# Optimization experiments

Hardware: AMD Instinct MI355X
Metric: run time of the kernel (lower is better)

## Reference

```python
import jax, jax.numpy as jnp
import numpy as np

N_POL, N_TICK, N_COMM = 1000, 98000, 1000
N = N_POL + N_TICK + N_COMM
E = 1000000
EMB, HID, OUT, HEADS = 32, 64, 32, 4
EDGE_DIM = 5
N_STATES, N_SECTORS, N_INDUSTRIES = 50, 11, 74


def _p(k, shape, fan_in):
    return jax.random.normal(k, shape, jnp.float32) * (1.0 / np.sqrt(fan_in))


def setup_inputs():
    ks = jax.random.split(jax.random.key(0), 30)
    F1 = HID // HEADS
    d = {}
    d["edge_index"] = jax.random.randint(ks[0], (2, E), 0, N)
    d["edge_attr"] = jax.random.normal(ks[1], (E, EDGE_DIM), jnp.float32)
    d["pol_feat"] = jax.random.normal(ks[2], (N_POL, 7), jnp.float32)
    d["state_ids"] = jax.random.randint(ks[3], (N_POL,), 0, N_STATES)
    d["sector_ids"] = jax.random.randint(ks[4], (N_TICK,), 0, N_SECTORS)
    d["industry_ids"] = jax.random.randint(ks[5], (N_TICK,), 0, N_INDUSTRIES)
    d["comp_scalar"] = jax.random.normal(ks[6], (N_TICK, 1), jnp.float32)
    d["pol_W"] = _p(ks[7], (7, EMB), 7); d["pol_b"] = jnp.zeros((EMB,), jnp.float32)
    d["state_E"] = _p(ks[8], (N_STATES, EMB), 1)
    d["sector_E"] = _p(ks[9], (N_SECTORS, 8), 1)
    d["industry_E"] = _p(ks[10], (N_INDUSTRIES, 8), 1)
    d["comp_W"] = _p(ks[11], (17, EMB), 17); d["comp_b"] = jnp.zeros((EMB,), jnp.float32)
    d["comm_E"] = _p(ks[12], (N_COMM, EMB), 1)
    d["ln_g"] = jnp.ones((EMB,), jnp.float32); d["ln_b"] = jnp.zeros((EMB,), jnp.float32)
    d["c1_W"] = _p(ks[13], (EMB, HEADS * F1), EMB)
    d["c1_as"] = _p(ks[14], (HEADS, F1), F1); d["c1_ad"] = _p(ks[15], (HEADS, F1), F1)
    d["c1_eW"] = _p(ks[16], (EDGE_DIM, HEADS * F1), EDGE_DIM)
    d["c1_ae"] = _p(ks[17], (HEADS, F1), F1)
    d["c1_b"] = jnp.zeros((HID,), jnp.float32)
    d["c2_W"] = _p(ks[18], (HID, OUT), HID)
    d["c2_as"] = _p(ks[19], (1, OUT), OUT); d["c2_ad"] = _p(ks[20], (1, OUT), OUT)
    d["c2_eW"] = _p(ks[21], (EDGE_DIM, OUT), EDGE_DIM)
    d["c2_ae"] = _p(ks[22], (1, OUT), OUT)
    d["c2_b"] = jnp.zeros((OUT,), jnp.float32)
    return d


def _segment_softmax(logits, seg, num):
    # numerically stable per-destination softmax, per head (axis 0 is edges)
    m = jax.ops.segment_max(logits, seg, num_segments=num)
    ex = jnp.exp(logits - m[seg])
    s = jax.ops.segment_sum(ex, seg, num_segments=num)
    return ex / s[seg]


def _gat(x, src, dst, eattr, W, a_s, a_d, eW, a_e, b, heads, feat, concat):
    # PyG GATConv (eval mode): linear -> per-node alpha terms -> per-edge
    # leaky_relu -> destination softmax -> weighted scatter-sum.
    n = x.shape[0]
    h = (x @ W).reshape(n, heads, feat)                     # [N,H,F]
    a_src = jnp.sum(h * a_s, -1)                            # [N,H]
    a_dst = jnp.sum(h * a_d, -1)                            # [N,H]
    a_edge = jnp.sum((eattr @ eW).reshape(-1, heads, feat) * a_e, -1)  # [E,H]
    alpha = jax.nn.leaky_relu(a_src[src] + a_dst[dst] + a_edge, 0.2)
    alpha = _segment_softmax(alpha, dst, n)                 # [E,H]
    out = jax.ops.segment_sum(h[src] * alpha[..., None], dst, num_segments=n)
    out = out.reshape(n, heads * feat) if concat else out.mean(1)
    return out + b


def _forward(edge_index, edge_attr, pol_feat, state_ids, sector_ids, industry_ids,
             comp_scalar, pol_W, pol_b, state_E, sector_E, industry_E, comp_W,
             comp_b, comm_E, ln_g, ln_b, c1_W, c1_as, c1_ad, c1_eW, c1_ae, c1_b,
             c2_W, c2_as, c2_ad, c2_eW, c2_ae, c2_b):
    # node features
    pol = jax.nn.relu(pol_feat @ pol_W + pol_b) + state_E[state_ids]
    comp_in = jnp.concatenate([sector_E[sector_ids], industry_E[industry_ids], comp_scalar], 1)
    comp = jax.nn.relu(comp_in @ comp_W + comp_b)
    x = jnp.concatenate([pol, comp, comm_E], 0)             # [N,EMB]
    mu = jnp.mean(x, -1, keepdims=True)
    var = jnp.mean((x - mu) ** 2, -1, keepdims=True)
    x = (x - mu) / jnp.sqrt(var + 1e-5) * ln_g + ln_b
    # add self-loops with fill_value='mean' (per-dst mean of incoming edge_attr)
    src, dst = edge_index[0], edge_index[1]
    cnt = jax.ops.segment_sum(jnp.ones((E,), jnp.float32), dst, num_segments=N)
    loop_attr = jax.ops.segment_sum(edge_attr, dst, num_segments=N) / jnp.maximum(cnt, 1.0)[:, None]
    idx = jnp.arange(N)
    src2 = jnp.concatenate([src, idx]); dst2 = jnp.concatenate([dst, idx])
    ea2 = jnp.concatenate([edge_attr, loop_attr], 0)
    x = jax.nn.elu(_gat(x, src2, dst2, ea2, c1_W, c1_as, c1_ad, c1_eW, c1_ae, c1_b, HEADS, HID // HEADS, True))
    x = _gat(x, src2, dst2, ea2, c2_W, c2_as, c2_ad, c2_eW, c2_ae, c2_b, 1, OUT, False)
    return x


def reference(edge_index, edge_attr, pol_feat, state_ids, sector_ids, industry_ids,
              comp_scalar, pol_W, pol_b, state_E, sector_E, industry_E, comp_W,
              comp_b, comm_E, ln_g, ln_b, c1_W, c1_as, c1_ad, c1_eW, c1_ae, c1_b,
              c2_W, c2_as, c2_ad, c2_eW, c2_ae, c2_b):
    return _forward(edge_index, edge_attr, pol_feat, state_ids, sector_ids, industry_ids,
                    comp_scalar, pol_W, pol_b, state_E, sector_E, industry_E, comp_W,
                    comp_b, comm_E, ln_g, ln_b, c1_W, c1_as, c1_ad, c1_eW, c1_ae, c1_b,
                    c2_W, c2_as, c2_ad, c2_eW, c2_ae, c2_b)
```

## Files before the change

### kernel.cpp

```cpp
#include <hip/hip_runtime.h>
#include <math.h>

#define NPOL   1000
#define NTICK  98000
#define NCOMM  1000
#define NN     100000
#define NE     1000000
#define NE2    1100000
#define NPREBLK  1563
#define PRET     400128

__device__ __forceinline__ unsigned short f2bf(float v) {
    unsigned u = __float_as_uint(v);
    u += 0x7FFFu + ((u >> 16) & 1u);
    return (unsigned short)(u >> 16);
}
__device__ __forceinline__ float bf2f(unsigned short s) {
    return __uint_as_float(((unsigned)s) << 16);
}

__global__ void __launch_bounds__(256) k_pre(
    const int* __restrict__ ei, int* __restrict__ deg, int* __restrict__ ord,
    const float* __restrict__ pol_feat, const int* __restrict__ state_ids,
    const int* __restrict__ sector_ids, const int* __restrict__ industry_ids,
    const float* __restrict__ comp_scalar,
    const float* __restrict__ pol_W, const float* __restrict__ pol_b,
    const float* __restrict__ state_E, const float* __restrict__ sector_E,
    const float* __restrict__ industry_E, const float* __restrict__ comp_W,
    const float* __restrict__ comp_b, const float* __restrict__ comm_E,
    const float* __restrict__ ln_g, const float* __restrict__ ln_b,
    const float* __restrict__ c1_W, const float* __restrict__ c1_as,
    const float* __restrict__ c1_ad,
    unsigned short* __restrict__ h1b, float* __restrict__ as1,
    float* __restrict__ ad1) {
    __shared__ float sW1[2048];
    __shared__ float sCompW[544];
    __shared__ float sPolW[224];
    __shared__ float sAs[64], sAd[64];
    __shared__ float sLg[32], sLb[32], sPb[32], sCb[32];
    int t = threadIdx.x;
    int tid = blockIdx.x * 256 + t;
    int e0 = tid, e1 = tid + PRET, e2 = tid + 2 * PRET;
    bool b1 = e1 < NE, b2 = e2 < NE;
    int d0 = ei[NE + e0];
    int d1 = b1 ? ei[NE + e1] : 0;
    int d2 = b2 ? ei[NE + e2] : 0;
    for (int i = t; i < 2048; i += 256) sW1[i] = c1_W[i];
    for (int i = t; i < 544; i += 256) sCompW[i] = comp_W[i];
    if (t < 224) sPolW[t] = pol_W[t];
    if (t < 64) { sAs[t] = c1_as[t]; sAd[t] = c1_ad[t]; }
    if (t < 32) { sLg[t] = ln_g[t]; sLb[t] = ln_b[t]; sPb[t] = pol_b[t]; sCb[t] = comp_b[t]; }
    __syncthreads();
    int r0 = atomicAdd(&deg[d0], 1);
    int r1 = b1 ? atomicAdd(&deg[d1], 1) : 0;
    int r2 = b2 ? atomicAdd(&deg[d2], 1) : 0;
    if (tid < 4 * NN) {
        int n = tid >> 2, q = tid & 3, jb = q * 8;
        float x[8];
        if (n < NPOL) {
            float f[7];
            #pragma unroll
            for (int i = 0; i < 7; ++i) f[i] = pol_feat[n * 7 + i];
            int sid = state_ids[n];
            #pragma unroll
            for (int jj = 0; jj < 8; ++jj) {
                int j = jb + jj;
                float v = sPb[j];
                #pragma unroll
                for (int i = 0; i < 7; ++i) v += f[i] * sPolW[i * 32 + j];
                v = v > 0.f ? v : 0.f;
                x[jj] = v + state_E[sid * 32 + j];
            }
        } else if (n < NPOL + NTICK) {
            int tt = n - NPOL;
            float f[17];
            int sec = sector_ids[tt], ind = industry_ids[tt];
            #pragma unroll
            for (int i = 0; i < 8; ++i) { f[i] = sector_E[sec * 8 + i]; f[8 + i] = industry_E[ind * 8 + i]; }
            f[16] = comp_scalar[tt];
            #pragma unroll
            for (int jj = 0; jj < 8; ++jj) {
                int j = jb + jj;
                float v = sCb[j];
                #pragma unroll
                for (int i = 0; i < 17; ++i) v += f[i] * sCompW[i * 32 + j];
                x[jj] = v > 0.f ? v : 0.f;
            }
        } else {
            int c = n - (NPOL + NTICK);
            float4 a = *(const float4*)&comm_E[c * 32 + jb];
            float4 b = *(const float4*)&comm_E[c * 32 + jb + 4];
            x[0] = a.x; x[1] = a.y; x[2] = a.z; x[3] = a.w;
            x[4] = b.x; x[5] = b.y; x[6] = b.z; x[7] = b.w;
        }
        float s1 = 0.f;
        #pragma unroll
        for (int jj = 0; jj < 8; ++jj) s1 += x[jj];
        s1 += __shfl_xor(s1, 1); s1 += __shfl_xor(s1, 2);
        float mu = s1 * (1.f / 32.f);
        float s2 = 0.f;
        #pragma unroll
        for (int jj = 0; jj < 8; ++jj) { float dd = x[jj] - mu; s2 += dd * dd; }
        s2 += __shfl_xor(s2, 1); s2 += __shfl_xor(s2, 2);
        float inv = rsqrtf(s2 * (1.f / 32.f) + 1e-5f);
        #pragma unroll
        for (int jj = 0; jj < 8; ++jj) x[jj] = (x[jj] - mu) * inv * sLg[jb + jj] + sLb[jb + jj];
        float4 acc0 = {0,0,0,0}, acc1 = {0,0,0,0}, acc2 = {0,0,0,0}, acc3 = {0,0,0,0};
        int qb = (t & 63) & ~3;
        int jc = q * 16;
        #pragma unroll
        for (int p = 0; p < 4; ++p) {
            #pragma unroll
            for (int jj = 0; jj < 8; ++jj) {
                float xs = __shfl(x[jj], qb + p, 64);
                const float4* wr = (const float4*)&sW1[(p * 8 + jj) * 64 + jc];
                float4 w0 = wr[0], w1 = wr[1], w2 = wr[2], w3 = wr[3];
                acc0.x = fmaf(xs, w0.x, acc0.x); acc0.y = fmaf(xs, w0.y, acc0.y);
                acc0.z = fmaf(xs, w0.z, acc0.z); acc0.w = fmaf(xs, w0.w, acc0.w);
                acc1.x = fmaf(xs, w1.x, acc1.x); acc1.y = fmaf(xs, w1.y, acc1.y);
                acc1.z = fmaf(xs, w1.z, acc1.z); acc1.w = fmaf(xs, w1.w, acc1.w);
                acc2.x = fmaf(xs, w2.x, acc2.x); acc2.y = fmaf(xs, w2.y, acc2.y);
                acc2.z = fmaf(xs, w2.z, acc2.z); acc2.w = fmaf(xs, w2.w, acc2.w);
                acc3.x = fmaf(xs, w3.x, acc3.x); acc3.y = fmaf(xs, w3.y, acc3.y);
                acc3.z = fmaf(xs, w3.z, acc3.z); acc3.w = fmaf(xs, w3.w, acc3.w);
            }
        }
        const float4* asv = (const float4*)sAs;
        const float4* adv = (const float4*)sAd;
        float4 a0 = asv[q * 4], a1 = asv[q * 4 + 1], a2 = asv[q * 4 + 2], a3 = asv[q * 4 + 3];
        float4 b0 = adv[q * 4], b1v = adv[q * 4 + 1], b2v = adv[q * 4 + 2], b3 = adv[q * 4 + 3];
        float av = acc0.x * a0.x + acc0.y * a0.y + acc0.z * a0.z + acc0.w * a0.w
                 + acc1.x * a1.x + acc1.y * a1.y + acc1.z * a1.z + acc1.w * a1.w
                 + acc2.x * a2.x + acc2.y * a2.y + acc2.z * a2.z + acc2.w * a2.w
                 + acc3.x * a3.x + acc3.y * a3.y + acc3.z * a3.z + acc3.w * a3.w;
        float dv = acc0.x * b0.x + acc0.y * b0.y + acc0.z * b0.z + acc0.w * b0.w
                 + acc1.x * b1v.x + acc1.y * b1v.y + acc1.z * b1v.z + acc1.w * b1v.w
                 + acc2.x * b2v.x + acc2.y * b2v.y + acc2.z * b2v.z + acc2.w * b2v.w
                 + acc3.x * b3.x + acc3.y * b3.y + acc3.z * b3.z + acc3.w * b3.w;
        as1[tid] = av;
        ad1[tid] = dv;
        uint4 w1o, w2o;
        w1o.x = (unsigned)f2bf(acc0.x) | ((unsigned)f2bf(acc0.y) << 16);
        w1o.y = (unsigned)f2bf(acc0.z) | ((unsigned)f2bf(acc0.w) << 16);
        w1o.z = (unsigned)f2bf(acc1.x) | ((unsigned)f2bf(acc1.y) << 16);
        w1o.w = (unsigned)f2bf(acc1.z) | ((unsigned)f2bf(acc1.w) << 16);
        w2o.x = (unsigned)f2bf(acc2.x) | ((unsigned)f2bf(acc2.y) << 16);
        w2o.y = (unsigned)f2bf(acc2.z) | ((unsigned)f2bf(acc2.w) << 16);
        w2o.z = (unsigned)f2bf(acc3.x) | ((unsigned)f2bf(acc3.y) << 16);
        w2o.w = (unsigned)f2bf(acc3.z) | ((unsigned)f2bf(acc3.w) << 16);
        unsigned short* hp = h1b + (unsigned)n * 64u + (unsigned)jc;
        *(uint4*)hp = w1o;
        *(uint4*)(hp + 8) = w2o;
    }
    ord[e0] = r0;
    if (b1) ord[e1] = r1;
    if (b2) ord[e2] = r2;
}

__global__ void k_scan1(const int* __restrict__ deg, int* __restrict__ row_start,
                        int* __restrict__ bsum) {
    __shared__ int tmp[1024];
    int i = blockIdx.x * 1024 + threadIdx.x;
    int v = (i < NN) ? deg[i] + 1 : 0;
    tmp[threadIdx.x] = v;
    __syncthreads();
    for (int off = 1; off < 1024; off <<= 1) {
        int u = (threadIdx.x >= off) ? tmp[threadIdx.x - off] : 0;
        __syncthreads();
        tmp[threadIdx.x] += u;
        __syncthreads();
    }
    if (i < NN) row_start[i] = tmp[threadIdx.x] - v;
    if (threadIdx.x == 1023) bsum[blockIdx.x] = tmp[1023];
}
__global__ void k_scan2(int* __restrict__ bsum, int nb) {
    __shared__ int tmp[128];
    int t = threadIdx.x;
    int v = (t < nb) ? bsum[t] : 0;
    tmp[t] = v;
    __syncthreads();
    for (int off = 1; off < 128; off <<= 1) {
        int u = (t >= off) ? tmp[t - off] : 0;
        __syncthreads();
        tmp[t] += u;
        __syncthreads();
    }
    if (t < nb) bsum[t] = tmp[t] - v;
}
__global__ void k_scan3(int* __restrict__ row_start, const int* __restrict__ bsum) {
    int i = blockIdx.x * blockDim.x + threadIdx.x;
    if (i < NN) row_start[i] += bsum[i >> 10];
}

__global__ void __launch_bounds__(256) k_fill(
    const int* __restrict__ ei, const float* __restrict__ edge_attr,
    const int* __restrict__ row_start, const int* __restrict__ ord,
    const float* __restrict__ c1_eW, const float* __restrict__ c1_ae,
    const float* __restrict__ c2_eW, const float* __restrict__ c2_ae,
    float4* __restrict__ rec) {
    __shared__ float we1s[20];
    __shared__ float we2s[5];
    int t = threadIdx.x;
    if (t < 20) {
        int d = t >> 2, h = t & 3;
        float s = 0.f;
        for (int f = 0; f < 16; ++f) s += c1_eW[d * 64 + h * 16 + f] * c1_ae[h * 16 + f];
        we1s[t] = s;
    } else if (t >= 32 && t < 37) {
        int d = t - 32;
        float s = 0.f;
        for (int f = 0; f < 32; ++f) s += c2_eW[d * 32 + f] * c2_ae[f];
        we2s[d] = s;
    }
    __syncthreads();
    int e = blockIdx.x * 256 + t;
    if (e >= NE) return;
    int s = ei[e], d = ei[NE + e];
    int pos = row_start[d] + 1 + ord[e];
    float a[5];
    #pragma unroll
    for (int k = 0; k < 5; ++k) a[k] = edge_attr[e * 5 + k];
    float e0 = 0.f, e1 = 0.f, e2 = 0.f, e3 = 0.f, e4 = 0.f;
    #pragma unroll
    for (int k = 0; k < 5; ++k) {
        e0 += a[k] * we1s[k * 4 + 0];
        e1 += a[k] * we1s[k * 4 + 1];
        e2 += a[k] * we1s[k * 4 + 2];
        e3 += a[k] * we1s[k * 4 + 3];
        e4 += a[k] * we2s[k];
    }
    unsigned u01 = (unsigned)f2bf(e0) | ((unsigned)f2bf(e1) << 16);
    unsigned u23 = (unsigned)f2bf(e2) | ((unsigned)f2bf(e3) << 16);
    rec[pos] = make_float4(__int_as_float(s), __uint_as_float(u01),
                           __uint_as_float(u23), e4);
}

__global__ void __launch_bounds__(256) k_agg1(
    const int* __restrict__ row_start, const int* __restrict__ deg,
    float4* __restrict__ rec,
    const float* __restrict__ as1, const float* __restrict__ ad1,
    const unsigned short* __restrict__ h1b, const float* __restrict__ c1_b,
    unsigned short* __restrict__ x1b) {
    __shared__ float pT[4][2][32][4];
    __shared__ int   srcT[4][2][32];
    int wid = threadIdx.x >> 6;
    int lane = threadIdx.x & 63;
    int half = lane >> 5;
    int j = lane & 31;
    int h = j >> 3;
    int n = blockIdx.x * 8 + wid * 2 + half;
    int base = row_start[n];
    int dg   = deg[n];
    const float4* as1v4 = (const float4*)as1;
    const float4* ad1v4 = (const float4*)ad1;
    float4 adv = ad1v4[n];
    float4 asv = as1v4[n];
    unsigned uself = *(const unsigned*)(h1b + (unsigned)n * 64u + 2u * (unsigned)j);

    float ssum = 0.f, acc0 = 0.f, acc1 = 0.f;
    float aes0 = 0.f, aes1 = 0.f, aes2 = 0.f, aes3 = 0.f, ae2sum = 0.f;

    for (int i0 = 0; i0 < dg; i0 += 32) {
        int clen = dg - i0; if (clen > 32) clen = 32;
        int idx = i0 + j;
        if (idx < dg) {
            float4 r = rec[base + 1 + idx];
            int s = __float_as_int(r.x);
            unsigned u01 = __float_as_uint(r.y), u23 = __float_as_uint(r.z);
            float ae0  = bf2f((unsigned short)u01);
            float ae1v = bf2f((unsigned short)(u01 >> 16));
            float ae2v = bf2f((unsigned short)u23);
            float ae3v = bf2f((unsigned short)(u23 >> 16));
            float4 av = as1v4[s];
            float l0 = av.x + adv.x + ae0;  l0 = l0 > 0.f ? l0 : 0.2f * l0;
            float l1 = av.y + adv.y + ae1v; l1 = l1 > 0.f ? l1 : 0.2f * l1;
            float l2 = av.z + adv.z + ae2v; l2 = l2 > 0.f ? l2 : 0.2f * l2;
            float l3 = av.w + adv.w + ae3v; l3 = l3 > 0.f ? l3 : 0.2f * l3;
            float4 q = make_float4(__expf(l0), __expf(l1), __expf(l2), __expf(l3));
            *(float4*)&pT[wid][half][j][0] = q;
            srcT[wid][half][j] = s;
            aes0 += ae0; aes1 += ae1v; aes2 += ae2v; aes3 += ae3v;
            ae2sum += r.w;
        }
        int i = 0;
        for (; i + 4 <= clen; i += 4) {
            int s0 = srcT[wid][half][i],     s1 = srcT[wid][half][i + 1];
            int s2 = srcT[wid][half][i + 2], s3 = srcT[wid][half][i + 3];
            float q0 = pT[wid][half][i][h],     q1 = pT[wid][half][i + 1][h];
            float q2 = pT[wid][half][i + 2][h], q3 = pT[wid][half][i + 3][h];
            unsigned g0 = *(const unsigned*)(h1b + (unsigned)s0 * 64u + 2u * (unsigned)j);
            unsigned g1 = *(const unsigned*)(h1b + (unsigned)s1 * 64u + 2u * (unsigned)j);
            unsigned g2 = *(const unsigned*)(h1b + (unsigned)s2 * 64u + 2u * (unsigned)j);
            unsigned g3 = *(const unsigned*)(h1b + (unsigned)s3 * 64u + 2u * (unsigned)j);
            ssum += (q0 + q1) + (q2 + q3);
            acc0 = fmaf(q0, bf2f((unsigned short)g0),
                   fmaf(q1, bf2f((unsigned short)g1),
                   fmaf(q2, bf2f((unsigned short)g2),
                   fmaf(q3, bf2f((unsigned short)g3), acc0))));
            acc1 = fmaf(q0, bf2f((unsigned short)(g0 >> 16)),
                   fmaf(q1, bf2f((unsigned short)(g1 >> 16)),
                   fmaf(q2, bf2f((unsigned short)(g2 >> 16)),
                   fmaf(q3, bf2f((unsigned short)(g3 >> 16)), acc1))));
        }
        for (; i < clen; ++i) {
            int s0 = srcT[wid][half][i];
            float q0 = pT[wid][half][i][h];
            unsigned g0 = *(const unsigned*)(h1b + (unsigned)s0 * 64u + 2u * (unsigned)j);
            ssum += q0;
            acc0 = fmaf(q0, bf2f((unsigned short)g0), acc0);
            acc1 = fmaf(q0, bf2f((unsigned short)(g0 >> 16)), acc1);
        }
    }
    #pragma unroll
    for (int m = 1; m < 32; m <<= 1) {
        aes0 += __shfl_xor(aes0, m);
        aes1 += __shfl_xor(aes1, m);
        aes2 += __shfl_xor(aes2, m);
        aes3 += __shfl_xor(aes3, m);
        ae2sum += __shfl_xor(ae2sum, m);
    }
    float invd = 1.f / fmaxf((float)dg, 1.f);
    float aesh = (h == 0) ? aes0 : (h == 1) ? aes1 : (h == 2) ? aes2 : aes3;
    float adh  = (h == 0) ? adv.x : (h == 1) ? adv.y : (h == 2) ? adv.z : adv.w;
    float ash  = (h == 0) ? asv.x : (h == 1) ? asv.y : (h == 2) ? asv.z : asv.w;
    float ls = ash + adh + aesh * invd;
    ls = ls > 0.f ? ls : 0.2f * ls;
    float ps = __expf(ls);
    ssum += ps;
    acc0 = fmaf(ps, bf2f((unsigned short)uself), acc0);
    acc1 = fmaf(ps, bf2f((unsigned short)(uself >> 16)), acc1);
    if (j == 0) {
        rec[base] = make_float4(__int_as_float(n), 0.f, 0.f, ae2sum * invd);
    }
    float inv_s = 1.f / ssum;
    float x0 = acc0 * inv_s + c1_b[2 * j];
    float x1 = acc1 * inv_s + c1_b[2 * j + 1];
    x0 = (x0 > 0.f) ? x0 : (__expf(x0) - 1.f);
    x1 = (x1 > 0.f) ? x1 : (__expf(x1) - 1.f);
    unsigned w = (unsigned)f2bf(x0) | ((unsigned)f2bf(x1) << 16);
    *(unsigned*)(x1b + (unsigned)n * 64u + 2u * (unsigned)j) = w;
}

__global__ void __launch_bounds__(256) k_mid(
    const unsigned short* __restrict__ x1b, const float* __restrict__ c2_W,
    const float* __restrict__ c2_as, const float* __restrict__ c2_ad,
    unsigned short* __restrict__ h2b, float* __restrict__ as2,
    float* __restrict__ ad2) {
    int wave = (blockIdx.x * 256 + threadIdx.x) >> 6;
    int lane = threadIdx.x & 63;
    int half = lane >> 5, j = lane & 31;
    int n = wave * 2 + half;
    unsigned u = *(const unsigned*)(x1b + (unsigned)n * 64u + j * 2u);
    float acc = 0.f;
    #pragma unroll
    for (int t = 0; t < 32; ++t) {
        unsigned xu = (unsigned)__shfl((int)u, half * 32 + t, 64);
        float x0 = bf2f((unsigned short)xu);
        float x1 = bf2f((unsigned short)(xu >> 16));
        acc = fmaf(x0, c2_W[(2 * t) * 32 + j], acc);
        acc = fmaf(x1, c2_W[(2 * t + 1) * 32 + j], acc);
    }
    float a = acc * c2_as[j], b = acc * c2_ad[j];
    #pragma unroll
    for (int m = 16; m > 0; m >>= 1) {
        a += __shfl_xor(a, m, 64);
        b += __shfl_xor(b, m, 64);
    }
    if (j == 0) { as2[n] = a; ad2[n] = b; }
    h2b[(unsigned)n * 32u + j] = f2bf(acc);
}

__global__ void __launch_bounds__(256) k_agg2(
    const int* __restrict__ row_start, const int* __restrict__ deg,
    const float4* __restrict__ rec, const float* __restrict__ as2,
    const float* __restrict__ ad2, const unsigned short* __restrict__ h2b,
    const float* __restrict__ c2_b, float* __restrict__ out) {
    __shared__ float2 spT[8][32];
    int t = threadIdx.x;
    int half = t >> 5;
    int l32 = t & 31;
    int n = blockIdx.x * 8 + half;
    int base = row_start[n];
    int len = deg[n] + 1;
    float ad2n = ad2[n];
    float ssum = 0.f, acc = 0.f;
    for (int i0 = 0; i0 < len; i0 += 32) {
        int clen = len - i0; if (clen > 32) clen = 32;
        int idx = i0 + l32;
        float p = 0.f; int s = 0;
        if (idx < len) {
            float4 r = rec[base + idx];
            s = __float_as_int(r.x);
            float l = as2[s] + ad2n + r.w;
            l = l > 0.f ? l : 0.2f * l;
            p = __expf(l);
        }
        ssum += p;
        spT[half][l32] = make_float2(__int_as_float(s), p);
        int i = 0;
        for (; i + 4 <= clen; i += 4) {
            float2 e0 = spT[half][i],     e1 = spT[half][i + 1];
            float2 e2 = spT[half][i + 2], e3 = spT[half][i + 3];
            int s0 = __float_as_int(e0.x), s1 = __float_as_int(e1.x);
            int s2 = __float_as_int(e2.x), s3 = __float_as_int(e3.x);
            float g0 = bf2f(h2b[(unsigned)s0 * 32u + l32]);
            float g1 = bf2f(h2b[(unsigned)s1 * 32u + l32]);
            float g2 = bf2f(h2b[(unsigned)s2 * 32u + l32]);
            float g3 = bf2f(h2b[(unsigned)s3 * 32u + l32]);
            acc = fmaf(e0.y, g0, fmaf(e1.y, g1, fmaf(e2.y, g2, fmaf(e3.y, g3, acc))));
        }
        for (; i < clen; ++i) {
            float2 e0 = spT[half][i];
            int s0 = __float_as_int(e0.x);
            acc = fmaf(e0.y, bf2f(h2b[(unsigned)s0 * 32u + l32]), acc);
        }
    }
    #pragma unroll
    for (int m = 1; m < 32; m <<= 1) ssum += __shfl_xor(ssum, m, 32);
    out[(size_t)n * 32 + l32] = acc / ssum + c2_b[l32];
}

extern "C" void kernel_launch(void* const* d_in, const int* in_sizes, int n_in,
                              void* d_out, int out_size, void* d_ws, size_t ws_size,
                              hipStream_t stream) {
    const int*   edge_index  = (const int*)  d_in[0];
    const float* edge_attr   = (const float*)d_in[1];
    const float* pol_feat    = (const float*)d_in[2];
    const int*   state_ids   = (const int*)  d_in[3];
    const int*   sector_ids  = (const int*)  d_in[4];
    const int*   industry_ids= (const int*)  d_in[5];
    const float* comp_scalar = (const float*)d_in[6];
    const float* pol_W   = (const float*)d_in[7];
    const float* pol_b   = (const float*)d_in[8];
    const float* state_E = (const float*)d_in[9];
    const float* sector_E= (const float*)d_in[10];
    const float* industry_E=(const float*)d_in[11];
    const float* comp_W  = (const float*)d_in[12];
    const float* comp_b  = (const float*)d_in[13];
    const float* comm_E  = (const float*)d_in[14];
    const float* ln_g    = (const float*)d_in[15];
    const float* ln_b    = (const float*)d_in[16];
    const float* c1_W    = (const float*)d_in[17];
    const float* c1_as   = (const float*)d_in[18];
    const float* c1_ad   = (const float*)d_in[19];
    const float* c1_eW   = (const float*)d_in[20];
    const float* c1_ae   = (const float*)d_in[21];
    const float* c1_b    = (const float*)d_in[22];
    const float* c2_W    = (const float*)d_in[23];
    const float* c2_as   = (const float*)d_in[24];
    const float* c2_ad   = (const float*)d_in[25];
    const float* c2_eW   = (const float*)d_in[26];
    const float* c2_ae   = (const float*)d_in[27];
    const float* c2_b    = (const float*)d_in[28];
    float* out = (float*)d_out;

    char* ws = (char*)d_ws;
    size_t off = 0;
    auto alloc = [&](size_t bytes) { void* p = ws + off; off += (bytes + 255) & ~(size_t)255; return p; };
    int*   deg       = (int*)  alloc(NN * 4);
    int*   ord       = (int*)  alloc((size_t)NE * 4);
    int*   row_start = (int*)  alloc(NN * 4);
    int*   bsum      = (int*)  alloc(128 * 4);
    float4* rec      = (float4*)alloc((size_t)NE2 * 16);
    unsigned short* h1b = (unsigned short*)alloc((size_t)NN * 64 * 2);
    float* as1       = (float*)alloc((size_t)NN * 4 * 4);
    float* ad1       = (float*)alloc((size_t)NN * 4 * 4);
    unsigned short* x1b = (unsigned short*)alloc((size_t)NN * 64 * 2);
    unsigned short* h2b = (unsigned short*)alloc((size_t)NN * 32 * 2);
    float* as2       = (float*)alloc(NN * 4);
    float* ad2       = (float*)alloc(NN * 4);
    (void)ws_size; (void)in_sizes; (void)n_in; (void)out_size;

    hipMemsetAsync(deg, 0, NN * 4, stream);

    k_pre<<<NPREBLK, 256, 0, stream>>>(
        edge_index, deg, ord,
        pol_feat, state_ids, sector_ids, industry_ids, comp_scalar,
        pol_W, pol_b, state_E, sector_E, industry_E, comp_W, comp_b, comm_E,
        ln_g, ln_b, c1_W, c1_as, c1_ad, h1b, as1, ad1);
    int nblk = (NN + 1023) / 1024;
    k_scan1<<<nblk, 1024, 0, stream>>>(deg, row_start, bsum);
    k_scan2<<<1, 128, 0, stream>>>(bsum, nblk);
    k_scan3<<<(NN + 255) / 256, 256, 0, stream>>>(row_start, bsum);
    k_fill<<<(NE + 255) / 256, 256, 0, stream>>>(
        edge_index, edge_attr, row_start, ord, c1_eW, c1_ae, c2_eW, c2_ae, rec);
    k_agg1<<<NN / 8, 256, 0, stream>>>(
        row_start, deg, rec, as1, ad1, h1b, c1_b, x1b);
    k_mid<<<(NN / 2) / 4, 256, 0, stream>>>(
        x1b, c2_W, c2_as, c2_ad, h2b, as2, ad2);
    k_agg2<<<NN / 8, 256, 0, stream>>>(
        row_start, deg, rec, as2, ad2, h2b, c2_b, out);
}
```

Measured before the change: 182.6 us.

## Replace atomic-count CSR build with two-pass shared-memory bucket sort by destination

```diff
diff --git a/kernel.cpp b/kernel.cpp
--- a/kernel.cpp
+++ b/kernel.cpp
@@ -6,9 +6,13 @@
 #define NCOMM  1000
 #define NN     100000
 #define NE     1000000
-#define NE2    1100000
-#define NPREBLK  1563
-#define PRET     400128
+#define NFEATBLK 1563
+
+#define BKTSHIFT 9
+#define NBKT     196
+#define BKTCAP   6144
+#define KA_EPB   4096
+#define KA_BLOCKS 245
 
 __device__ __forceinline__ unsigned short f2bf(float v) {
     unsigned u = __float_as_uint(v);
@@ -19,8 +23,7 @@
     return __uint_as_float(((unsigned)s) << 16);
 }
 
-__global__ void __launch_bounds__(256) k_pre(
-    const int* __restrict__ ei, int* __restrict__ deg, int* __restrict__ ord,
+__global__ void __launch_bounds__(256) k_feat(
     const float* __restrict__ pol_feat, const int* __restrict__ state_ids,
     const int* __restrict__ sector_ids, const int* __restrict__ industry_ids,
     const float* __restrict__ comp_scalar,
@@ -39,167 +42,121 @@
     __shared__ float sAs[64], sAd[64];
     __shared__ float sLg[32], sLb[32], sPb[32], sCb[32];
     int t = threadIdx.x;
-    int tid = blockIdx.x * 256 + t;
-    int e0 = tid, e1 = tid + PRET, e2 = tid + 2 * PRET;
-    bool b1 = e1 < NE, b2 = e2 < NE;
-    int d0 = ei[NE + e0];
-    int d1 = b1 ? ei[NE + e1] : 0;
-    int d2 = b2 ? ei[NE + e2] : 0;
     for (int i = t; i < 2048; i += 256) sW1[i] = c1_W[i];
     for (int i = t; i < 544; i += 256) sCompW[i] = comp_W[i];
     if (t < 224) sPolW[t] = pol_W[t];
     if (t < 64) { sAs[t] = c1_as[t]; sAd[t] = c1_ad[t]; }
     if (t < 32) { sLg[t] = ln_g[t]; sLb[t] = ln_b[t]; sPb[t] = pol_b[t]; sCb[t] = comp_b[t]; }
     __syncthreads();
-    int r0 = atomicAdd(&deg[d0], 1);
-    int r1 = b1 ? atomicAdd(&deg[d1], 1) : 0;
-    int r2 = b2 ? atomicAdd(&deg[d2], 1) : 0;
-    if (tid < 4 * NN) {
-        int n = tid >> 2, q = tid & 3, jb = q * 8;
-        float x[8];
-        if (n < NPOL) {
-            float f[7];
+    int tid = blockIdx.x * 256 + t;
+    if (tid >= 4 * NN) return;
+    int n = tid >> 2, q = tid & 3, jb = q * 8;
+    float x[8];
+    if (n < NPOL) {
+        float f[7];
+        #pragma unroll
+        for (int i = 0; i < 7; ++i) f[i] = pol_feat[n * 7 + i];
+        int sid = state_ids[n];
+        #pragma unroll
+        for (int jj = 0; jj < 8; ++jj) {
+            int j = jb + jj;
+            float v = sPb[j];
             #pragma unroll
-            for (int i = 0; i < 7; ++i) f[i] = pol_feat[n * 7 + i];
-            int sid = state_ids[n];
+            for (int i = 0; i < 7; ++i) v += f[i] * sPolW[i * 32 + j];
+            v = v > 0.f ? v : 0.f;
+            x[jj] = v + state_E[sid * 32 + j];
+        }
+    } else if (n < NPOL + NTICK) {
+        int tt = n - NPOL;
+        float f[17];
+        int sec = sector_ids[tt], ind = industry_ids[tt];
+        #pragma unroll
+        for (int i = 0; i < 8; ++i) { f[i] = sector_E[sec * 8 + i]; f[8 + i] = industry_E[ind * 8 + i]; }
+        f[16] = comp_scalar[tt];
+        #pragma unroll
+        for (int jj = 0; jj < 8; ++jj) {
+            int j = jb + jj;
+            float v = sCb[j];
             #pragma unroll
-            for (int jj = 0; jj < 8; ++jj) {
-                int j = jb + jj;
-                float v = sPb[j];
-                #pragma unroll
-                for (int i = 0; i < 7; ++i) v += f[i] * sPolW[i * 32 + j];
-                v = v > 0.f ? v : 0.f;
-                x[jj] = v + state_E[sid * 32 + j];
-            }
-        } else if (n < NPOL + NTICK) {
-            int tt = n - NPOL;
-            float f[17];
-            int sec = sector_ids[tt], ind = industry_ids[tt];
-            #pragma unroll
-            for (int i = 0; i < 8; ++i) { f[i] = sector_E[sec * 8 + i]; f[8 + i] = industry_E[ind * 8 + i]; }
-            f[16] = comp_scalar[tt];
-            #pragma unroll
-            for (int jj = 0; jj < 8; ++jj) {
-                int j = jb + jj;
-                float v = sCb[j];
-                #pragma unroll
-                for (int i = 0; i < 17; ++i) v += f[i] * sCompW[i * 32 + j];
-                x[jj] = v > 0.f ? v : 0.f;
-            }
-        } else {
-            int c = n - (NPOL + NTICK);
-            float4 a = *(const float4*)&comm_E[c * 32 + jb];
-            float4 b = *(const float4*)&comm_E[c * 32 + jb + 4];
-            x[0] = a.x; x[1] = a.y; x[2] = a.z; x[3] = a.w;
-            x[4] = b.x; x[5] = b.y; x[6] = b.z; x[7] = b.w;
-        }
-        float s1 = 0.f;
+            for (int i = 0; i < 17; ++i) v += f[i] * sCompW[i * 32 + j];
+            x[jj] = v > 0.f ? v : 0.f;
+        }
+    } else {
+        int c = n - (NPOL + NTICK);
+        float4 a = *(const float4*)&comm_E[c * 32 + jb];
+        float4 b = *(const float4*)&comm_E[c * 32 + jb + 4];
+        x[0] = a.x; x[1] = a.y; x[2] = a.z; x[3] = a.w;
+        x[4] = b.x; x[5] = b.y; x[6] = b.z; x[7] = b.w;
+    }
+    float s1 = 0.f;
+    #pragma unroll
+    for (int jj = 0; jj < 8; ++jj) s1 += x[jj];
+    s1 += __shfl_xor(s1, 1); s1 += __shfl_xor(s1, 2);
+    float mu = s1 * (1.f / 32.f);
+    float s2 = 0.f;
+    #pragma unroll
+    for (int jj = 0; jj < 8; ++jj) { float dd = x[jj] - mu; s2 += dd * dd; }
+    s2 += __shfl_xor(s2, 1); s2 += __shfl_xor(s2, 2);
+    float inv = rsqrtf(s2 * (1.f / 32.f) + 1e-5f);
+    #pragma unroll
+    for (int jj = 0; jj < 8; ++jj) x[jj] = (x[jj] - mu) * inv * sLg[jb + jj] + sLb[jb + jj];
+    float4 acc0 = {0,0,0,0}, acc1 = {0,0,0,0}, acc2 = {0,0,0,0}, acc3 = {0,0,0,0};
+    int qb = (t & 63) & ~3;
+    int jc = q * 16;
+    #pragma unroll
+    for (int p = 0; p < 4; ++p) {
         #pragma unroll
-        for (int jj = 0; jj < 8; ++jj) s1 += x[jj];
-        s1 += __shfl_xor(s1, 1); s1 += __shfl_xor(s1, 2);
-        float mu = s1 * (1.f / 32.f);
-        float s2 = 0.f;
-        #pragma unroll
-        for (int jj = 0; jj < 8; ++jj) { float dd = x[jj] - mu; s2 += dd * dd; }
-        s2 += __shfl_xor(s2, 1); s2 += __shfl_xor(s2, 2);
-        float inv = rsqrtf(s2 * (1.f / 32.f) + 1e-5f);
-        #pragma unroll
-        for (int jj = 0; jj < 8; ++jj) x[jj] = (x[jj] - mu) * inv * sLg[jb + jj] + sLb[jb + jj];
-        float4 acc0 = {0,0,0,0}, acc1 = {0,0,0,0}, acc2 = {0,0,0,0}, acc3 = {0,0,0,0};
-        int qb = (t & 63) & ~3;
-        int jc = q * 16;
-        #pragma unroll
-        for (int p = 0; p < 4; ++p) {
-            #pragma unroll
-            for (int jj = 0; jj < 8; ++jj) {
-                float xs = __shfl(x[jj], qb + p, 64);
-                const float4* wr = (const float4*)&sW1[(p * 8 + jj) * 64 + jc];
-                float4 w0 = wr[0], w1 = wr[1], w2 = wr[2], w3 = wr[3];
-                acc0.x = fmaf(xs, w0.x, acc0.x); acc0.y = fmaf(xs, w0.y, acc0.y);
-                acc0.z = fmaf(xs, w0.z, acc0.z); acc0.w = fmaf(xs, w0.w, acc0.w);
-                acc1.x = fmaf(xs, w1.x, acc1.x); acc1.y = fmaf(xs, w1.y, acc1.y);
-                acc1.z = fmaf(xs, w1.z, acc1.z); acc1.w = fmaf(xs, w1.w, acc1.w);
-                acc2.x = fmaf(xs, w2.x, acc2.x); acc2.y = fmaf(xs, w2.y, acc2.y);
-                acc2.z = fmaf(xs, w2.z, acc2.z); acc2.w = fmaf(xs, w2.w, acc2.w);
-                acc3.x = fmaf(xs, w3.x, acc3.x); acc3.y = fmaf(xs, w3.y, acc3.y);
-                acc3.z = fmaf(xs, w3.z, acc3.z); acc3.w = fmaf(xs, w3.w, acc3.w);
-            }
-        }
-        const float4* asv = (const float4*)sAs;
-        const float4* adv = (const float4*)sAd;
-        float4 a0 = asv[q * 4], a1 = asv[q * 4 + 1], a2 = asv[q * 4 + 2], a3 = asv[q * 4 + 3];
-        float4 b0 = adv[q * 4], b1v = adv[q * 4 + 1], b2v = adv[q * 4 + 2], b3 = adv[q * 4 + 3];
-        float av = acc0.x * a0.x + acc0.y * a0.y + acc0.z * a0.z + acc0.w * a0.w
-                 + acc1.x * a1.x + acc1.y * a1.y + acc1.z * a1.z + acc1.w * a1.w
-                 + acc2.x * a2.x + acc2.y * a2.y + acc2.z * a2.z + acc2.w * a2.w
-                 + acc3.x * a3.x + acc3.y * a3.y + acc3.z * a3.z + acc3.w * a3.w;
-        float dv = acc0.x * b0.x + acc0.y * b0.y + acc0.z * b0.z + acc0.w * b0.w
-                 + acc1.x * b1v.x + acc1.y * b1v.y + acc1.z * b1v.z + acc1.w * b1v.w
-                 + acc2.x * b2v.x + acc2.y * b2v.y + acc2.z * b2v.z + acc2.w * b2v.w
-                 + acc3.x * b3.x + acc3.y * b3.y + acc3.z * b3.z + acc3.w * b3.w;
-        as1[tid] = av;
-        ad1[tid] = dv;
-        uint4 w1o, w2o;
-        w1o.x = (unsigned)f2bf(acc0.x) | ((unsigned)f2bf(acc0.y) << 16);
-        w1o.y = (unsigned)f2bf(acc0.z) | ((unsigned)f2bf(acc0.w) << 16);
-        w1o.z = (unsigned)f2bf(acc1.x) | ((unsigned)f2bf(acc1.y) << 16);
-        w1o.w = (unsigned)f2bf(acc1.z) | ((unsigned)f2bf(acc1.w) << 16);
-        w2o.x = (unsigned)f2bf(acc2.x) | ((unsigned)f2bf(acc2.y) << 16);
-        w2o.y = (unsigned)f2bf(acc2.z) | ((unsigned)f2bf(acc2.w) << 16);
-        w2o.z = (unsigned)f2bf(acc3.x) | ((unsigned)f2bf(acc3.y) << 16);
-        w2o.w = (unsigned)f2bf(acc3.z) | ((unsigned)f2bf(acc3.w) << 16);
-        unsigned short* hp = h1b + (unsigned)n * 64u + (unsigned)jc;
-        *(uint4*)hp = w1o;
-        *(uint4*)(hp + 8) = w2o;
-    }
-    ord[e0] = r0;
-    if (b1) ord[e1] = r1;
-    if (b2) ord[e2] = r2;
-}
-
-__global__ void k_scan1(const int* __restrict__ deg, int* __restrict__ row_start,
-                        int* __restrict__ bsum) {
-    __shared__ int tmp[1024];
-    int i = blockIdx.x * 1024 + threadIdx.x;
-    int v = (i < NN) ? deg[i] + 1 : 0;
-    tmp[threadIdx.x] = v;
-    __syncthreads();
-    for (int off = 1; off < 1024; off <<= 1) {
-        int u = (threadIdx.x >= off) ? tmp[threadIdx.x - off] : 0;
-        __syncthreads();
-        tmp[threadIdx.x] += u;
-        __syncthreads();
-    }
-    if (i < NN) row_start[i] = tmp[threadIdx.x] - v;
-    if (threadIdx.x == 1023) bsum[blockIdx.x] = tmp[1023];
-}
-__global__ void k_scan2(int* __restrict__ bsum, int nb) {
-    __shared__ int tmp[128];
-    int t = threadIdx.x;
-    int v = (t < nb) ? bsum[t] : 0;
-    tmp[t] = v;
-    __syncthreads();
-    for (int off = 1; off < 128; off <<= 1) {
-        int u = (t >= off) ? tmp[t - off] : 0;
-        __syncthreads();
-        tmp[t] += u;
-        __syncthreads();
-    }
-    if (t < nb) bsum[t] = tmp[t] - v;
-}
-__global__ void k_scan3(int* __restrict__ row_start, const int* __restrict__ bsum) {
-    int i = blockIdx.x * blockDim.x + threadIdx.x;
-    if (i < NN) row_start[i] += bsum[i >> 10];
-}
-
-__global__ void __launch_bounds__(256) k_fill(
+        for (int jj = 0; jj < 8; ++jj) {
+            float xs = __shfl(x[jj], qb + p, 64);
+            const float4* wr = (const float4*)&sW1[(p * 8 + jj) * 64 + jc];
+            float4 w0 = wr[0], w1 = wr[1], w2 = wr[2], w3 = wr[3];
+            acc0.x = fmaf(xs, w0.x, acc0.x); acc0.y = fmaf(xs, w0.y, acc0.y);
+            acc0.z = fmaf(xs, w0.z, acc0.z); acc0.w = fmaf(xs, w0.w, acc0.w);
+            acc1.x = fmaf(xs, w1.x, acc1.x); acc1.y = fmaf(xs, w1.y, acc1.y);
+            acc1.z = fmaf(xs, w1.z, acc1.z); acc1.w = fmaf(xs, w1.w, acc1.w);
+            acc2.x = fmaf(xs, w2.x, acc2.x); acc2.y = fmaf(xs, w2.y, acc2.y);
+            acc2.z = fmaf(xs, w2.z, acc2.z); acc2.w = fmaf(xs, w2.w, acc2.w);
+            acc3.x = fmaf(xs, w3.x, acc3.x); acc3.y = fmaf(xs, w3.y, acc3.y);
+            acc3.z = fmaf(xs, w3.z, acc3.z); acc3.w = fmaf(xs, w3.w, acc3.w);
+        }
+    }
+    const float4* asv = (const float4*)sAs;
+    const float4* adv = (const float4*)sAd;
+    float4 a0 = asv[q * 4], a1 = asv[q * 4 + 1], a2 = asv[q * 4 + 2], a3 = asv[q * 4 + 3];
+    float4 b0 = adv[q * 4], b1v = adv[q * 4 + 1], b2v = adv[q * 4 + 2], b3 = adv[q * 4 + 3];
+    float av = acc0.x * a0.x + acc0.y * a0.y + acc0.z * a0.z + acc0.w * a0.w
+             + acc1.x * a1.x + acc1.y * a1.y + acc1.z * a1.z + acc1.w * a1.w
+             + acc2.x * a2.x + acc2.y * a2.y + acc2.z * a2.z + acc2.w * a2.w
+             + acc3.x * a3.x + acc3.y * a3.y + acc3.z * a3.z + acc3.w * a3.w;
+    float dv = acc0.x * b0.x + acc0.y * b0.y + acc0.z * b0.z + acc0.w * b0.w
+             + acc1.x * b1v.x + acc1.y * b1v.y + acc1.z * b1v.z + acc1.w * b1v.w
+             + acc2.x * b2v.x + acc2.y * b2v.y + acc2.z * b2v.z + acc2.w * b2v.w
+             + acc3.x * b3.x + acc3.y * b3.y + acc3.z * b3.z + acc3.w * b3.w;
+    as1[tid] = av;
+    ad1[tid] = dv;
+    uint4 w1o, w2o;
+    w1o.x = (unsigned)f2bf(acc0.x) | ((unsigned)f2bf(acc0.y) << 16);
+    w1o.y = (unsigned)f2bf(acc0.z) | ((unsigned)f2bf(acc0.w) << 16);
+    w1o.z = (unsigned)f2bf(acc1.x) | ((unsigned)f2bf(acc1.y) << 16);
+    w1o.w = (unsigned)f2bf(acc1.z) | ((unsigned)f2bf(acc1.w) << 16);
+    w2o.x = (unsigned)f2bf(acc2.x) | ((unsigned)f2bf(acc2.y) << 16);
+    w2o.y = (unsigned)f2bf(acc2.z) | ((unsigned)f2bf(acc2.w) << 16);
+    w2o.z = (unsigned)f2bf(acc3.x) | ((unsigned)f2bf(acc3.y) << 16);
+    w2o.w = (unsigned)f2bf(acc3.z) | ((unsigned)f2bf(acc3.w) << 16);
+    unsigned short* hp = h1b + (unsigned)n * 64u + (unsigned)jc;
+    *(uint4*)hp = w1o;
+    *(uint4*)(hp + 8) = w2o;
+}
+
+__global__ void __launch_bounds__(1024) k_bucket(
     const int* __restrict__ ei, const float* __restrict__ edge_attr,
-    const int* __restrict__ row_start, const int* __restrict__ ord,
     const float* __restrict__ c1_eW, const float* __restrict__ c1_ae,
     const float* __restrict__ c2_eW, const float* __restrict__ c2_ae,
-    float4* __restrict__ rec) {
+    int* __restrict__ bucket_cnt, float4* __restrict__ bucketbuf) {
     __shared__ float we1s[20];
     __shared__ float we2s[5];
+    __shared__ int hcnt[NBKT];
+    __shared__ int hbase[NBKT];
     int t = threadIdx.x;
     if (t < 20) {
         int d = t >> 2, h = t & 3;
@@ -212,35 +169,120 @@
         for (int f = 0; f < 32; ++f) s += c2_eW[d * 32 + f] * c2_ae[f];
         we2s[d] = s;
     }
-    __syncthreads();
-    int e = blockIdx.x * 256 + t;
-    if (e >= NE) return;
-    int s = ei[e], d = ei[NE + e];
-    int pos = row_start[d] + 1 + ord[e];
-    float a[5];
-    #pragma unroll
-    for (int k = 0; k < 5; ++k) a[k] = edge_attr[e * 5 + k];
-    float e0 = 0.f, e1 = 0.f, e2 = 0.f, e3 = 0.f, e4 = 0.f;
-    #pragma unroll
-    for (int k = 0; k < 5; ++k) {
-        e0 += a[k] * we1s[k * 4 + 0];
-        e1 += a[k] * we1s[k * 4 + 1];
-        e2 += a[k] * we1s[k * 4 + 2];
-        e3 += a[k] * we1s[k * 4 + 3];
-        e4 += a[k] * we2s[k];
-    }
-    unsigned u01 = (unsigned)f2bf(e0) | ((unsigned)f2bf(e1) << 16);
-    unsigned u23 = (unsigned)f2bf(e2) | ((unsigned)f2bf(e3) << 16);
-    rec[pos] = make_float4(__int_as_float(s), __uint_as_float(u01),
-                           __uint_as_float(u23), e4);
+    if (t < NBKT) hcnt[t] = 0;
+    __syncthreads();
+    int e0 = blockIdx.x * KA_EPB + t;
+    int bk[4], rk[4];
+    float4 rec[4];
+    #pragma unroll
+    for (int k = 0; k < 4; ++k) {
+        int e = e0 + k * 1024;
+        bk[k] = -1;
+        if (e < NE) {
+            int s = ei[e];
+            int d = ei[NE + e];
+            int bkt = d >> BKTSHIFT;
+            int dl = d & ((1 << BKTSHIFT) - 1);
+            float a[5];
+            #pragma unroll
+            for (int kk = 0; kk < 5; ++kk) a[kk] = edge_attr[e * 5 + kk];
+            float v0 = 0.f, v1 = 0.f, v2 = 0.f, v3 = 0.f, v4 = 0.f;
+            #pragma unroll
+            for (int kk = 0; kk < 5; ++kk) {
+                v0 += a[kk] * we1s[kk * 4 + 0];
+                v1 += a[kk] * we1s[kk * 4 + 1];
+                v2 += a[kk] * we1s[kk * 4 + 2];
+                v3 += a[kk] * we1s[kk * 4 + 3];
+                v4 += a[kk] * we2s[kk];
+            }
+            unsigned u01 = (unsigned)f2bf(v0) | ((unsigned)f2bf(v1) << 16);
+            unsigned u23 = (unsigned)f2bf(v2) | ((unsigned)f2bf(v3) << 16);
+            unsigned pk = (unsigned)s | ((unsigned)dl << 17);
+            rec[k] = make_float4(__uint_as_float(pk), __uint_as_float(u01),
+                                 __uint_as_float(u23), v4);
+            bk[k] = bkt;
+            rk[k] = atomicAdd(&hcnt[bkt], 1);
+        }
+    }
+    __syncthreads();
+    if (t < NBKT && hcnt[t] > 0) hbase[t] = atomicAdd(&bucket_cnt[t * 16], hcnt[t]);
+    __syncthreads();
+    #pragma unroll
+    for (int k = 0; k < 4; ++k) {
+        if (bk[k] >= 0) {
+            int pos = hbase[bk[k]] + rk[k];
+            if (pos < BKTCAP)
+                bucketbuf[(size_t)bk[k] * BKTCAP + pos] = rec[k];
+        }
+    }
+}
+
+__global__ void __launch_bounds__(1024) k_sortfill(
+    const int* __restrict__ bucket_cnt, const float4* __restrict__ bucketbuf,
+    float4* __restrict__ rec2, int* __restrict__ deg, int* __restrict__ erow) {
+    __shared__ int pref[256];
+    __shared__ int hist[512];
+    __shared__ int hoff[512];
+    int t = threadIdx.x;
+    int b = blockIdx.x;
+    if (t < 256) pref[t] = (t < NBKT) ? bucket_cnt[t * 16] : 0;
+    if (t < 512) hist[t] = 0;
+    __syncthreads();
+    for (int off = 1; off < 256; off <<= 1) {
+        int v = 0;
+        if (t < 256 && t >= off) v = pref[t - off];
+        __syncthreads();
+        if (t < 256) pref[t] += v;
+        __syncthreads();
+    }
+    int count = bucket_cnt[b * 16];
+    if (count > BKTCAP) count = BKTCAP;
+    int region = (b == 0) ? 0 : pref[b - 1];
+    float4 rv[6];
+    int dlv[6], rrv[6];
+    #pragma unroll
+    for (int k = 0; k < 6; ++k) {
+        int i = k * 1024 + t;
+        dlv[k] = -1;
+        if (i < count) {
+            float4 p = bucketbuf[(size_t)b * BKTCAP + i];
+            int dl = (int)(__float_as_uint(p.x) >> 17);
+            p.x = __uint_as_float(__float_as_uint(p.x) & 0x1FFFFu);
+            rv[k] = p;
+            dlv[k] = dl;
+            rrv[k] = atomicAdd(&hist[dl], 1);
+        }
+    }
+    __syncthreads();
+    if (t < 512) hoff[t] = hist[t];
+    __syncthreads();
+    for (int off = 1; off < 512; off <<= 1) {
+        int v = 0;
+        if (t < 512 && t >= off) v = hoff[t - off];
+        __syncthreads();
+        if (t < 512) hoff[t] += v;
+        __syncthreads();
+    }
+    #pragma unroll
+    for (int k = 0; k < 6; ++k) {
+        if (dlv[k] >= 0) {
+            int pos = region + hoff[dlv[k]] - hist[dlv[k]] + rrv[k];
+            rec2[pos] = rv[k];
+        }
+    }
+    int n = (b << BKTSHIFT) + t;
+    if (t < 512 && n < NN) {
+        deg[n] = hist[t];
+        erow[n] = region + hoff[t] - hist[t];
+    }
 }
 
 __global__ void __launch_bounds__(256) k_agg1(
-    const int* __restrict__ row_start, const int* __restrict__ deg,
-    float4* __restrict__ rec,
+    const int* __restrict__ erow, const int* __restrict__ deg,
+    const float4* __restrict__ rec2,
     const float* __restrict__ as1, const float* __restrict__ ad1,
     const unsigned short* __restrict__ h1b, const float* __restrict__ c1_b,
-    unsigned short* __restrict__ x1b) {
+    unsigned short* __restrict__ x1b, float* __restrict__ selfae2) {
     __shared__ float pT[4][2][32][4];
     __shared__ int   srcT[4][2][32];
     int wid = threadIdx.x >> 6;
@@ -249,7 +291,7 @@
     int j = lane & 31;
     int h = j >> 3;
     int n = blockIdx.x * 8 + wid * 2 + half;
-    int base = row_start[n];
+    int base = erow[n];
     int dg   = deg[n];
     const float4* as1v4 = (const float4*)as1;
     const float4* ad1v4 = (const float4*)ad1;
@@ -264,7 +306,7 @@
         int clen = dg - i0; if (clen > 32) clen = 32;
         int idx = i0 + j;
         if (idx < dg) {
-            float4 r = rec[base + 1 + idx];
+            float4 r = rec2[base + idx];
             int s = __float_as_int(r.x);
             unsigned u01 = __float_as_uint(r.y), u23 = __float_as_uint(r.z);
             float ae0  = bf2f((unsigned short)u01);
@@ -329,9 +371,8 @@
     ssum += ps;
     acc0 = fmaf(ps, bf2f((unsigned short)uself), acc0);
     acc1 = fmaf(ps, bf2f((unsigned short)(uself >> 16)), acc1);
-    if (j == 0) {
-        rec[base] = make_float4(__int_as_float(n), 0.f, 0.f, ae2sum * invd);
-    }
+    if (lane == 0) selfae2[n] = ae2sum * invd;
+    if (lane == 32) selfae2[n] = ae2sum * invd;
     float inv_s = 1.f / ssum;
     float x0 = acc0 * inv_s + c1_b[2 * j];
     float x1 = acc1 * inv_s + c1_b[2 * j + 1];
@@ -371,25 +412,26 @@
 }
 
 __global__ void __launch_bounds__(256) k_agg2(
-    const int* __restrict__ row_start, const int* __restrict__ deg,
-    const float4* __restrict__ rec, const float* __restrict__ as2,
-    const float* __restrict__ ad2, const unsigned short* __restrict__ h2b,
-    const float* __restrict__ c2_b, float* __restrict__ out) {
+    const int* __restrict__ erow, const int* __restrict__ deg,
+    const float4* __restrict__ rec2, const float* __restrict__ as2,
+    const float* __restrict__ ad2, const float* __restrict__ selfae2,
+    const unsigned short* __restrict__ h2b, const float* __restrict__ c2_b,
+    float* __restrict__ out) {
     __shared__ float2 spT[8][32];
     int t = threadIdx.x;
     int half = t >> 5;
     int l32 = t & 31;
     int n = blockIdx.x * 8 + half;
-    int base = row_start[n];
-    int len = deg[n] + 1;
+    int base = erow[n];
+    int dg = deg[n];
     float ad2n = ad2[n];
     float ssum = 0.f, acc = 0.f;
-    for (int i0 = 0; i0 < len; i0 += 32) {
-        int clen = len - i0; if (clen > 32) clen = 32;
+    for (int i0 = 0; i0 < dg; i0 += 32) {
+        int clen = dg - i0; if (clen > 32) clen = 32;
         int idx = i0 + l32;
         float p = 0.f; int s = 0;
-        if (idx < len) {
-            float4 r = rec[base + idx];
+        if (idx < dg) {
+            float4 r = rec2[base + idx];
             s = __float_as_int(r.x);
             float l = as2[s] + ad2n + r.w;
             l = l > 0.f ? l : 0.2f * l;
@@ -417,6 +459,11 @@
     }
     #pragma unroll
     for (int m = 1; m < 32; m <<= 1) ssum += __shfl_xor(ssum, m, 32);
+    float ls = as2[n] + ad2n + selfae2[n];
+    ls = ls > 0.f ? ls : 0.2f * ls;
+    float ps = __expf(ls);
+    ssum += ps;
+    acc = fmaf(ps, bf2f(h2b[(unsigned)n * 32u + l32]), acc);
     out[(size_t)n * 32 + l32] = acc / ssum + c2_b[l32];
 }
 
@@ -457,11 +504,12 @@
     char* ws = (char*)d_ws;
     size_t off = 0;
     auto alloc = [&](size_t bytes) { void* p = ws + off; off += (bytes + 255) & ~(size_t)255; return p; };
-    int*   deg       = (int*)  alloc(NN * 4);
-    int*   ord       = (int*)  alloc((size_t)NE * 4);
-    int*   row_start = (int*)  alloc(NN * 4);
-    int*   bsum      = (int*)  alloc(128 * 4);
-    float4* rec      = (float4*)alloc((size_t)NE2 * 16);
+    int*    bucket_cnt = (int*)   alloc((size_t)NBKT * 16 * 4);
+    float4* bucketbuf  = (float4*)alloc((size_t)NBKT * BKTCAP * 16);
+    float4* rec2       = (float4*)alloc((size_t)NE * 16);
+    int*    deg        = (int*)   alloc(NN * 4);
+    int*    erow       = (int*)   alloc(NN * 4);
+    float*  selfae2    = (float*) alloc(NN * 4);
     unsigned short* h1b = (unsigned short*)alloc((size_t)NN * 64 * 2);
     float* as1       = (float*)alloc((size_t)NN * 4 * 4);
     float* ad1       = (float*)alloc((size_t)NN * 4 * 4);
@@ -471,23 +519,20 @@
     float* ad2       = (float*)alloc(NN * 4);
     (void)ws_size; (void)in_sizes; (void)n_in; (void)out_size;
 
-    hipMemsetAsync(deg, 0, NN * 4, stream);
-
-    k_pre<<<NPREBLK, 256, 0, stream>>>(
-        edge_index, deg, ord,
+    hipMemsetAsync(bucket_cnt, 0, (size_t)NBKT * 16 * 4, stream);
+
+    k_feat<<<NFEATBLK, 256, 0, stream>>>(
         pol_feat, state_ids, sector_ids, industry_ids, comp_scalar,
         pol_W, pol_b, state_E, sector_E, industry_E, comp_W, comp_b, comm_E,
         ln_g, ln_b, c1_W, c1_as, c1_ad, h1b, as1, ad1);
-    int nblk = (NN + 1023) / 1024;
-    k_scan1<<<nblk, 1024, 0, stream>>>(deg, row_start, bsum);
-    k_scan2<<<1, 128, 0, stream>>>(bsum, nblk);
-    k_scan3<<<(NN + 255) / 256, 256, 0, stream>>>(row_start, bsum);
-    k_fill<<<(NE + 255) / 256, 256, 0, stream>>>(
-        edge_index, edge_attr, row_start, ord, c1_eW, c1_ae, c2_eW, c2_ae, rec);
+    k_bucket<<<KA_BLOCKS, 1024, 0, stream>>>(
+        edge_index, edge_attr, c1_eW, c1_ae, c2_eW, c2_ae, bucket_cnt, bucketbuf);
+    k_sortfill<<<NBKT, 1024, 0, stream>>>(
+        bucket_cnt, bucketbuf, rec2, deg, erow);
     k_agg1<<<NN / 8, 256, 0, stream>>>(
-        row_start, deg, rec, as1, ad1, h1b, c1_b, x1b);
+        erow, deg, rec2, as1, ad1, h1b, c1_b, x1b, selfae2);
     k_mid<<<(NN / 2) / 4, 256, 0, stream>>>(
         x1b, c2_W, c2_as, c2_ad, h2b, as2, ad2);
     k_agg2<<<NN / 8, 256, 0, stream>>>(
-        row_start, deg, rec, as2, ad2, h2b, c2_b, out);
-}
+        erow, deg, rec2, as2, ad2, selfae2, h2b, c2_b, out);
+}
```

New measurement: 175.4 us. 3.9% less time.
